# Optimization experiments

Hardware: AMD Instinct MI355X
Metric: run time of the kernel (lower is better)

## Reference

```python
import jax, jax.numpy as jnp
import numpy as np

DIM = 4096
N_HEADS = 32
HEAD_DIM = DIM // N_HEADS  # 128
B = 2
S = 2048
ADAPTER_LEN = 10
NEG_INF = -1e30


def _rope(t, cos, sin):
    # t: [B, S, H, hd]; cos/sin: [S, hd//2]
    b, s, h, d = t.shape
    tr = t.reshape(b, s, h, d // 2, 2)
    a, bb = tr[..., 0], tr[..., 1]
    c = cos[None, :, None, :]
    sn = sin[None, :, None, :]
    out = jnp.stack([a * c - bb * sn, a * sn + bb * c], axis=-1)
    return out.reshape(b, s, h, d)


def _attn(q, k, v, mask=None):
    # q: [B,H,Q,d], k/v: [B,H,K,d]
    scores = jnp.einsum('bhqd,bhkd->bhqk', q, k) / np.sqrt(HEAD_DIM).astype(q.dtype)
    if mask is not None:
        scores = scores + mask
    probs = jax.nn.softmax(scores.astype(jnp.float32), axis=-1).astype(q.dtype)
    return jnp.einsum('bhqk,bhkd->bhqd', probs, v)


def setup_inputs() -> dict:
    key = jax.random.key(0)
    ks = jax.random.split(key, 8)
    w_std = 0.02
    x = jax.random.normal(ks[0], (B, S, DIM), dtype=jnp.float32)
    wq = jax.random.normal(ks[1], (DIM, DIM), dtype=jnp.float32) * w_std
    wk = jax.random.normal(ks[2], (DIM, DIM), dtype=jnp.float32) * w_std
    wv = jax.random.normal(ks[3], (DIM, DIM), dtype=jnp.float32) * w_std
    wo = jax.random.normal(ks[4], (DIM, DIM), dtype=jnp.float32) * w_std
    gate = jax.random.normal(ks[5], (1, N_HEADS, 1, 1), dtype=jnp.float32)
    adapter = jax.random.normal(ks[6], (1, ADAPTER_LEN, DIM), dtype=jnp.float32)
    # RoPE tables (theta = 10000)
    inv_freq = 1.0 / (10000.0 ** (np.arange(0, HEAD_DIM, 2, dtype=np.float32) / HEAD_DIM))
    angles = np.outer(np.arange(S, dtype=np.float32), inv_freq)  # [S, hd//2]
    freqs_cos = jnp.asarray(np.cos(angles), dtype=jnp.float32)
    freqs_sin = jnp.asarray(np.sin(angles), dtype=jnp.float32)
    # causal additive mask [1,1,S,S]
    mask = jnp.triu(jnp.full((S, S), NEG_INF, dtype=jnp.float32), k=1)[None, None]
    return {"x": x, "wq": wq, "wk": wk, "wv": wv, "wo": wo, "gate": gate,
            "adapter": adapter, "freqs_cos": freqs_cos, "freqs_sin": freqs_sin,
            "mask": mask, "start_pos": 0}


def reference(x, wq, wk, wv, wo, gate, adapter, freqs_cos, freqs_sin, mask, start_pos):
    bsz, seqlen, _ = x.shape
    # QKV projections (torch Linear: y = x @ W.T)
    xq = jnp.einsum('bsd,ed->bse', x, wq).reshape(bsz, seqlen, N_HEADS, HEAD_DIM)
    xk = jnp.einsum('bsd,ed->bse', x, wk).reshape(bsz, seqlen, N_HEADS, HEAD_DIM)
    xv = jnp.einsum('bsd,ed->bse', x, wv).reshape(bsz, seqlen, N_HEADS, HEAD_DIM)
    xq = _rope(xq, freqs_cos, freqs_sin)
    xk = _rope(xk, freqs_cos, freqs_sin)
    # KV-cache write + read: start_pos == 0 and cache is zero-initialized, so
    # keys/values over [:start_pos+seqlen] equal the freshly written xk/xv.
    q = xq.transpose(0, 2, 1, 3)      # [B,H,S,d]
    keys = xk.transpose(0, 2, 1, 3)
    values = xv.transpose(0, 2, 1, 3)
    output = _attn(q, keys, values, mask)
    # gated adapter cross-attention
    a_k = jnp.einsum('bld,ed->ble', adapter, wk).reshape(1, ADAPTER_LEN, N_HEADS, HEAD_DIM)
    a_v = jnp.einsum('bld,ed->ble', adapter, wv).reshape(1, ADAPTER_LEN, N_HEADS, HEAD_DIM)
    a_k = jnp.broadcast_to(a_k, (bsz, ADAPTER_LEN, N_HEADS, HEAD_DIM)).transpose(0, 2, 1, 3)
    a_v = jnp.broadcast_to(a_v, (bsz, ADAPTER_LEN, N_HEADS, HEAD_DIM)).transpose(0, 2, 1, 3)
    output = output + jnp.tanh(gate) * _attn(q, a_k, a_v)
    output = output.transpose(0, 2, 1, 3).reshape(bsz, seqlen, DIM)
    return jnp.einsum('bse,de->bsd', output, wo)
```

## Files before the change

kernel.cpp:

```cpp
#include <hip/hip_runtime.h>

typedef unsigned short u16;
typedef __attribute__((ext_vector_type(8))) short short8;
typedef __attribute__((ext_vector_type(4))) float f32x4;

#define L2E   1.44269504088896340736f
#define SCALE 0.08838834764831845f
#define NEGI  -1e30f
#define WN    ((size_t)4096 * 4096)
#define TNB   ((size_t)2048 * 4096)

__device__ __forceinline__ float b2f(u16 u) {
  union { float f; unsigned int i; } v; v.i = ((unsigned int)u) << 16; return v.f;
}
__device__ __forceinline__ u16 f2b(float f) {
  union { float f; unsigned int i; } v; v.f = f;
  unsigned int r = v.i + 0x7fffu + ((v.i >> 16) & 1u);
  return (u16)(r >> 16);
}
__device__ __forceinline__ void gload16(const u16* g, u16* l) {
  __builtin_amdgcn_global_load_lds((const __attribute__((address_space(1))) void*)g,
                                   (__attribute__((address_space(3))) void*)l, 16, 0, 0);
}
__device__ __forceinline__ short8 ld8_f32_to_bf16(const float* p) {
  float4 a = *(const float4*)p;
  float4 b = *(const float4*)(p + 4);
  short8 pk;
  pk[0] = (short)f2b(a.x); pk[1] = (short)f2b(a.y);
  pk[2] = (short)f2b(a.z); pk[3] = (short)f2b(a.w);
  pk[4] = (short)f2b(b.x); pk[5] = (short)f2b(b.y);
  pk[6] = (short)f2b(b.z); pk[7] = (short)f2b(b.w);
  return pk;
}

__global__ __launch_bounds__(256) void cvt_bf16(const float* __restrict__ src,
                                                u16* __restrict__ dst)
{
  size_t e = ((size_t)blockIdx.x * 256 + threadIdx.x) * 8;
  *(short8*)(dst + e) = ld8_f32_to_bf16(src + e);
}

__global__ __launch_bounds__(256, 2) void gemm_nt(const u16* __restrict__ A,
    const u16* __restrict__ B, void* __restrict__ Cv, int mode)
{
  __shared__ __align__(16) u16 As[128 * 64];
  __shared__ __align__(16) u16 Bs[128 * 64];
  const int tid  = threadIdx.x;
  const int wave = tid >> 6, lane = tid & 63;
  const int quad = lane >> 4, l16 = lane & 15;
  const int bm = blockIdx.y * 128, bn = blockIdx.x * 128;
  const int wm = (wave >> 1) * 64, wn = (wave & 1) * 64;

  f32x4 acc[4][4];
#pragma unroll
  for (int i = 0; i < 4; i++)
#pragma unroll
    for (int j = 0; j < 4; j++) acc[i][j] = (f32x4)0.0f;

  for (int k0 = 0; k0 < 4096; k0 += 64) {
    __syncthreads();
#pragma unroll
    for (int i = 0; i < 4; i++) {
      int c = tid + i * 256;
      int row = c >> 3, cb = (c & 7) << 3;
      gload16(A + (((size_t)(bm + row)) << 12) + k0 + cb, As + c * 8);
      gload16(B + (((size_t)(bn + row)) << 12) + k0 + cb, Bs + c * 8);
    }
    __syncthreads();
#pragma unroll
    for (int ks = 0; ks < 2; ks++) {
      short8 af[4], bf[4];
#pragma unroll
      for (int t = 0; t < 4; t++) {
        af[t] = *(const short8*)(As + (wm + t * 16 + l16) * 64 + ks * 32 + quad * 8);
        bf[t] = *(const short8*)(Bs + (wn + t * 16 + l16) * 64 + ks * 32 + quad * 8);
      }
#pragma unroll
      for (int mt = 0; mt < 4; mt++)
#pragma unroll
        for (int nt = 0; nt < 4; nt++)
          acc[mt][nt] = __builtin_amdgcn_mfma_f32_16x16x32_bf16(af[mt], bf[nt], acc[mt][nt], 0, 0, 0);
    }
  }
#pragma unroll
  for (int mt = 0; mt < 4; mt++)
#pragma unroll
    for (int nt = 0; nt < 4; nt++)
#pragma unroll
      for (int r = 0; r < 4; r++) {
        int row = bm + wm + mt * 16 + quad * 4 + r;
        int col = bn + wn + nt * 16 + l16;
        float v = acc[mt][nt][r];
        if (mode == 2) {
          ((float*)Cv)[(((size_t)row) << 12) + col] = v;
        } else if (mode == 1) {
          ((u16*)Cv)[((size_t)(col >> 11)) * TNB + (((size_t)row) << 11) + (col & 2047)] = f2b(v);
        } else {
          ((u16*)Cv)[(((size_t)row) << 12) + col] = f2b(v);
        }
      }
}

__global__ __launch_bounds__(256) void rope_kernel(u16* __restrict__ Q, u16* __restrict__ K,
    const float* __restrict__ fc, const float* __restrict__ fs)
{
  int gid = blockIdx.x * 256 + threadIdx.x;
  int tsel = gid >> 21;
  int r = gid & 2097151;
  int row = r >> 9, gp = r & 511;
  int s = row & 2047;
  int e0 = gp * 8;
  int i0 = (e0 >> 1) & 63;
  u16* p = (tsel ? K : Q) + (((size_t)row) << 12) + e0;
  short8 v = *(const short8*)p;
  float4 c4 = *(const float4*)(fc + s * 64 + i0);
  float4 s4 = *(const float4*)(fs + s * 64 + i0);
  float cc[4] = {c4.x, c4.y, c4.z, c4.w};
  float ss[4] = {s4.x, s4.y, s4.z, s4.w};
  short8 w;
#pragma unroll
  for (int j = 0; j < 4; j++) {
    float a  = b2f((u16)v[2 * j]);
    float bb = b2f((u16)v[2 * j + 1]);
    w[2 * j]     = (short)f2b(a * cc[j] - bb * ss[j]);
    w[2 * j + 1] = (short)f2b(a * ss[j] + bb * cc[j]);
  }
  *(short8*)p = w;
}

__global__ __launch_bounds__(256) void adapter_kv(const float* __restrict__ adapter,
    const float* __restrict__ wk, const float* __restrict__ wv,
    u16* __restrict__ ak, u16* __restrict__ av)
{
  int gid  = blockIdx.x * 4 + (threadIdx.x >> 6);
  int lane = threadIdx.x & 63;
  int which = (gid >= 40960) ? 1 : 0;
  int rem = gid - which * 40960;
  int l = rem >> 12, col = rem & 4095;
  const float* w = which ? wv : wk;
  u16* o = which ? av : ak;
  const float* arow = adapter + l * 4096;
  const float* wrow = w + (((size_t)col) << 12);
  float sum = 0.f;
#pragma unroll
  for (int i = 0; i < 8; i++) {
    int e = i * 512 + lane * 8;
    float4 a0 = *(const float4*)(arow + e);
    float4 a1 = *(const float4*)(arow + e + 4);
    float4 w0 = *(const float4*)(wrow + e);
    float4 w1 = *(const float4*)(wrow + e + 4);
    sum += a0.x * w0.x + a0.y * w0.y + a0.z * w0.z + a0.w * w0.w
         + a1.x * w1.x + a1.y * w1.y + a1.z * w1.z + a1.w * w1.w;
  }
#pragma unroll
  for (int off = 1; off < 64; off <<= 1) sum += __shfl_xor(sum, off, 64);
  if (lane == 0) o[rem] = f2b(sum);
}

__global__ __launch_bounds__(256, 2) void flash_attn(const u16* __restrict__ Q,
    const u16* __restrict__ K, const u16* __restrict__ V, u16* __restrict__ O)
{
  Q += (size_t)blockIdx.y * TNB;
  K += (size_t)blockIdx.y * TNB;
  V += (size_t)blockIdx.y * TNB;
  O += (size_t)blockIdx.y * TNB;
  __shared__ __align__(16) u16 sm[40960];
  u16* Ps = sm + 32768;
  const int tid  = threadIdx.x;
  const int wave = tid >> 6, lane = tid & 63;
  const int quad = lane >> 4, l16 = lane & 15;
  const int qt = 15 - blockIdx.z;
  const int h  = blockIdx.x;
  const int q0 = qt * 128;
  const size_t qkBase = (size_t)h * 128;
  const size_t vBase  = ((size_t)(h * 128)) << 11;

  u16* Qs = sm + 16384;
#pragma unroll
  for (int i = 0; i < 8; i++) {
    int c = tid + i * 256;
    int row = c >> 4;
    int cb  = ((c & 15) ^ (row & 7)) << 3;
    gload16(Q + qkBase + (((size_t)(q0 + row)) << 12) + cb, Qs + c * 8);
  }
#pragma unroll
  for (int i = 0; i < 4; i++) {
    int c = tid + i * 256;
    int krow = c >> 4;
    int kcb  = ((c & 15) ^ (krow & 7)) << 3;
    gload16(K + qkBase + (((size_t)krow) << 12) + kcb, sm + c * 8);
    int vrow = c >> 3;
    int vcb  = ((c & 7) ^ (vrow & 7)) << 3;
    gload16(V + vBase + (((size_t)vrow) << 11) + vcb, sm + 8192 + c * 8);
  }
  __syncthreads();
  short8 qa[2][4];
#pragma unroll
  for (int mt = 0; mt < 2; mt++)
#pragma unroll
    for (int ks = 0; ks < 4; ks++) {
      int qr = wave * 32 + mt * 16 + l16;
      qa[mt][ks] = *(const short8*)(Qs + qr * 128 + (((ks * 4 + quad) ^ (qr & 7)) << 3));
    }
  __syncthreads();

  f32x4 acc_o[2][8];
#pragma unroll
  for (int mt = 0; mt < 2; mt++)
#pragma unroll
    for (int n = 0; n < 8; n++) acc_o[mt][n] = (f32x4)0.0f;
  float m_st[2][4], l_st[2][4];
#pragma unroll
  for (int mt = 0; mt < 2; mt++)
#pragma unroll
    for (int r = 0; r < 4; r++) { m_st[mt][r] = NEGI; l_st[mt][r] = 0.f; }

  const int qw0 = q0 + wave * 32;
  const int ntiles = 2 * (qt + 1);
  for (int t = 0; t < ntiles; t++) {
    const int kv0 = t * 64;
    u16* Kc = sm + (t & 1) * 16384;
    u16* Vc = Kc + 8192;
    if (t + 1 < ntiles) {
      const int nk = kv0 + 64;
      u16* Kn = sm + ((t + 1) & 1) * 16384;
      u16* Vn = Kn + 8192;
#pragma unroll
      for (int i = 0; i < 4; i++) {
        int c = tid + i * 256;
        int krow = c >> 4;
        int kcb  = ((c & 15) ^ (krow & 7)) << 3;
        gload16(K + qkBase + (((size_t)(nk + krow)) << 12) + kcb, Kn + c * 8);
        int vrow = c >> 3;
        int vcb  = ((c & 7) ^ (vrow & 7)) << 3;
        gload16(V + vBase + (((size_t)vrow) << 11) + nk + vcb, Vn + c * 8);
      }
    }

    if (kv0 <= qw0 + 31) {
      f32x4 sc[2][4];
#pragma unroll
      for (int mt = 0; mt < 2; mt++)
#pragma unroll
        for (int nt = 0; nt < 4; nt++) sc[mt][nt] = (f32x4)0.0f;
      __builtin_amdgcn_s_setprio(1);
#pragma unroll
      for (int ks = 0; ks < 4; ks++) {
        short8 kb[4];
#pragma unroll
        for (int nt = 0; nt < 4; nt++) {
          int kr = nt * 16 + l16;
          kb[nt] = *(const short8*)(Kc + kr * 128 + (((ks * 4 + quad) ^ (kr & 7)) << 3));
        }
#pragma unroll
        for (int mt = 0; mt < 2; mt++)
#pragma unroll
          for (int nt = 0; nt < 4; nt++)
            sc[mt][nt] = __builtin_amdgcn_mfma_f32_16x16x32_bf16(qa[mt][ks], kb[nt], sc[mt][nt], 0, 0, 0);
      }
      __builtin_amdgcn_s_setprio(0);
#pragma unroll
      for (int mt = 0; mt < 2; mt++)
#pragma unroll
        for (int nt = 0; nt < 4; nt++)
#pragma unroll
          for (int r = 0; r < 4; r++) {
            int qrow = qw0 + mt * 16 + quad * 4 + r;
            int key  = kv0 + nt * 16 + l16;
            float s = sc[mt][nt][r] * SCALE;
            sc[mt][nt][r] = (key > qrow) ? NEGI : s;
          }
      float alpha[2][4];
#pragma unroll
      for (int mt = 0; mt < 2; mt++)
#pragma unroll
        for (int r = 0; r < 4; r++) {
          float mx = fmaxf(fmaxf(sc[mt][0][r], sc[mt][1][r]), fmaxf(sc[mt][2][r], sc[mt][3][r]));
          mx = fmaxf(mx, __shfl_xor(mx, 1, 64));
          mx = fmaxf(mx, __shfl_xor(mx, 2, 64));
          mx = fmaxf(mx, __shfl_xor(mx, 4, 64));
          mx = fmaxf(mx, __shfl_xor(mx, 8, 64));
          float mnew = fmaxf(m_st[mt][r], mx);
          float al = __builtin_amdgcn_exp2f((m_st[mt][r] - mnew) * L2E);
          float rs = 0.f;
#pragma unroll
          for (int nt = 0; nt < 4; nt++) {
            float p = __builtin_amdgcn_exp2f((sc[mt][nt][r] - mnew) * L2E);
            sc[mt][nt][r] = p;
            rs += p;
          }
          rs += __shfl_xor(rs, 1, 64);
          rs += __shfl_xor(rs, 2, 64);
          rs += __shfl_xor(rs, 4, 64);
          rs += __shfl_xor(rs, 8, 64);
          l_st[mt][r] = l_st[mt][r] * al + rs;
          m_st[mt][r] = mnew;
          alpha[mt][r] = al;
        }
#pragma unroll
      for (int mt = 0; mt < 2; mt++)
#pragma unroll
        for (int n = 0; n < 8; n++)
#pragma unroll
          for (int r = 0; r < 4; r++) acc_o[mt][n][r] *= alpha[mt][r];
      u16* Pw = Ps + wave * 2048;
#pragma unroll
      for (int mt = 0; mt < 2; mt++)
#pragma unroll
        for (int nt = 0; nt < 4; nt++)
#pragma unroll
          for (int r = 0; r < 4; r++) {
            int prow = mt * 16 + quad * 4 + r;
            int pcol = nt * 16 + l16;
            Pw[prow * 64 + (((pcol >> 3) ^ (prow & 7)) << 3) + (pcol & 7)] = f2b(sc[mt][nt][r]);
          }
      __builtin_amdgcn_s_setprio(1);
#pragma unroll
      for (int ks2 = 0; ks2 < 2; ks2++) {
        short8 pa[2];
#pragma unroll
        for (int mt = 0; mt < 2; mt++) {
          int pr = mt * 16 + l16;
          pa[mt] = *(const short8*)(Pw + pr * 64 + (((ks2 * 4 + quad) ^ (pr & 7)) << 3));
        }
#pragma unroll
        for (int n = 0; n < 8; n++) {
          int vr = n * 16 + l16;
          short8 vb = *(const short8*)(Vc + vr * 64 + (((ks2 * 4 + quad) ^ (vr & 7)) << 3));
#pragma unroll
          for (int mt = 0; mt < 2; mt++)
            acc_o[mt][n] = __builtin_amdgcn_mfma_f32_16x16x32_bf16(pa[mt], vb, acc_o[mt][n], 0, 0, 0);
        }
      }
      __builtin_amdgcn_s_setprio(0);
    }
    __syncthreads();
  }
#pragma unroll
  for (int mt = 0; mt < 2; mt++)
#pragma unroll
    for (int r = 0; r < 4; r++) {
      float inv = 1.0f / l_st[mt][r];
      int qrow = qw0 + mt * 16 + quad * 4 + r;
#pragma unroll
      for (int n = 0; n < 8; n++) {
        int d = n * 16 + l16;
        O[qkBase + (((size_t)qrow) << 12) + d] = f2b(acc_o[mt][n][r] * inv);
      }
    }
}

__global__ __launch_bounds__(256) void adapter_attn(const u16* __restrict__ Q,
    const u16* __restrict__ ak, const u16* __restrict__ av,
    const float* __restrict__ gate, u16* __restrict__ AO)
{
  int gid  = blockIdx.x * 4 + (threadIdx.x >> 6);
  int lane = threadIdx.x & 63;
  int row = gid >> 5, h = gid & 31;
  float g = tanhf(gate[h]);
  const u16* qp = Q + (((size_t)row) << 12) + h * 128 + lane * 2;
  float qa = b2f(qp[0]), qb = b2f(qp[1]);
  float p[10];
#pragma unroll
  for (int l = 0; l < 10; l++) {
    const u16* kp = ak + l * 4096 + h * 128 + lane * 2;
    p[l] = qa * b2f(kp[0]) + qb * b2f(kp[1]);
  }
#pragma unroll
  for (int l = 0; l < 10; l++)
#pragma unroll
    for (int off = 1; off < 64; off <<= 1) p[l] += __shfl_xor(p[l], off, 64);
  float m = NEGI;
#pragma unroll
  for (int l = 0; l < 10; l++) { p[l] *= SCALE; m = fmaxf(m, p[l]); }
  float sum = 0.f;
#pragma unroll
  for (int l = 0; l < 10; l++) { p[l] = __builtin_amdgcn_exp2f((p[l] - m) * L2E); sum += p[l]; }
  float gi = g / sum;
  float a0 = 0.f, a1 = 0.f;
#pragma unroll
  for (int l = 0; l < 10; l++) {
    const u16* vp = av + l * 4096 + h * 128 + lane * 2;
    a0 += p[l] * b2f(vp[0]);
    a1 += p[l] * b2f(vp[1]);
  }
  u16* op = AO + (((size_t)row) << 12) + h * 128 + lane * 2;
  op[0] = f2b(b2f(op[0]) + gi * a0);
  op[1] = f2b(b2f(op[1]) + gi * a1);
}

extern "C" void kernel_launch(void* const* d_in, const int* in_sizes, int n_in,
                              void* d_out, int out_size, void* d_ws, size_t ws_size,
                              hipStream_t stream) {
  (void)in_sizes; (void)n_in; (void)out_size; (void)ws_size;
  const float* x       = (const float*)d_in[0];
  const float* wq      = (const float*)d_in[1];
  const float* wk      = (const float*)d_in[2];
  const float* wv      = (const float*)d_in[3];
  const float* wo      = (const float*)d_in[4];
  const float* gate    = (const float*)d_in[5];
  const float* adapter = (const float*)d_in[6];
  const float* fc      = (const float*)d_in[7];
  const float* fs      = (const float*)d_in[8];
  float* out = (float*)d_out;

  u16* wb  = (u16*)d_ws;
  u16* xb  = wb + WN;
  u16* Qf  = xb + WN;
  u16* Kf  = Qf + WN;
  u16* Vtf = Kf + WN;
  u16* AOf = xb;
  u16* ak  = Vtf + WN;
  u16* av  = ak + 40960;

  adapter_kv<<<20480, 256, 0, stream>>>(adapter, wk, wv, ak, av);
  cvt_bf16<<<8192, 256, 0, stream>>>(x, xb);

  cvt_bf16<<<8192, 256, 0, stream>>>(wq, wb);
  gemm_nt<<<dim3(32, 32), 256, 0, stream>>>(xb, wb, Qf, 0);
  cvt_bf16<<<8192, 256, 0, stream>>>(wk, wb);
  gemm_nt<<<dim3(32, 32), 256, 0, stream>>>(xb, wb, Kf, 0);
  cvt_bf16<<<8192, 256, 0, stream>>>(wv, wb);
  gemm_nt<<<dim3(32, 32), 256, 0, stream>>>(wb, xb, Vtf, 1);

  rope_kernel<<<16384, 256, 0, stream>>>(Qf, Kf, fc, fs);
  flash_attn<<<dim3(32, 2, 16), 256, 0, stream>>>(Qf, Kf, Vtf, AOf);
  adapter_attn<<<32768, 256, 0, stream>>>(Qf, ak, av, gate, AOf);

  cvt_bf16<<<8192, 256, 0, stream>>>(wo, wb);
  gemm_nt<<<dim3(32, 32), 256, 0, stream>>>(AOf, wb, out, 2);
}
```

Measured before the change: 1.488 ms.

## Double-buffer GEMM LDS tiles and XOR-swizzle to avoid bank conflicts

The bf16 NT GEMM now uses two LDS buffers per operand, issuing global-to-LDS loads for the next K tile while MFMAs run on the current one. A single barrier per iteration replaces the two. The LDS column chunks are also XOR-swizzled by row so the 16-byte fragment reads spread across banks. LDS use doubles to 64KB per block, which may limit the intended two blocks per CU. Correctness depends on the vmcnt wait placed before the barrier covering the async loads.

```diff
diff --git a/kernel.cpp b/kernel.cpp
--- a/kernel.cpp
+++ b/kernel.cpp
@@ -43,8 +43,8 @@
 __global__ __launch_bounds__(256, 2) void gemm_nt(const u16* __restrict__ A,
     const u16* __restrict__ B, void* __restrict__ Cv, int mode)
 {
-  __shared__ __align__(16) u16 As[128 * 64];
-  __shared__ __align__(16) u16 Bs[128 * 64];
+  __shared__ __align__(16) u16 As[2][128 * 64];
+  __shared__ __align__(16) u16 Bs[2][128 * 64];
   const int tid  = threadIdx.x;
   const int wave = tid >> 6, lane = tid & 63;
   const int quad = lane >> 4, l16 = lane & 15;
@@ -57,23 +57,38 @@
 #pragma unroll
     for (int j = 0; j < 4; j++) acc[i][j] = (f32x4)0.0f;
 
-  for (int k0 = 0; k0 < 4096; k0 += 64) {
-    __syncthreads();
-#pragma unroll
-    for (int i = 0; i < 4; i++) {
-      int c = tid + i * 256;
-      int row = c >> 3, cb = (c & 7) << 3;
-      gload16(A + (((size_t)(bm + row)) << 12) + k0 + cb, As + c * 8);
-      gload16(B + (((size_t)(bn + row)) << 12) + k0 + cb, Bs + c * 8);
-    }
-    __syncthreads();
+#pragma unroll
+  for (int i = 0; i < 4; i++) {
+    int c = tid + i * 256;
+    int row = c >> 3;
+    int cb  = ((c & 7) ^ (row & 7)) << 3;
+    gload16(A + (((size_t)(bm + row)) << 12) + cb, As[0] + c * 8);
+    gload16(B + (((size_t)(bn + row)) << 12) + cb, Bs[0] + c * 8);
+  }
+  __syncthreads();
+
+  for (int t = 0; t < 64; t++) {
+    const int bi = t & 1;
+    if (t < 63) {
+      const int k0 = (t + 1) * 64;
+#pragma unroll
+      for (int i = 0; i < 4; i++) {
+        int c = tid + i * 256;
+        int row = c >> 3;
+        int cb  = ((c & 7) ^ (row & 7)) << 3;
+        gload16(A + (((size_t)(bm + row)) << 12) + k0 + cb, As[bi ^ 1] + c * 8);
+        gload16(B + (((size_t)(bn + row)) << 12) + k0 + cb, Bs[bi ^ 1] + c * 8);
+      }
+    }
 #pragma unroll
     for (int ks = 0; ks < 2; ks++) {
       short8 af[4], bf[4];
 #pragma unroll
-      for (int t = 0; t < 4; t++) {
-        af[t] = *(const short8*)(As + (wm + t * 16 + l16) * 64 + ks * 32 + quad * 8);
-        bf[t] = *(const short8*)(Bs + (wn + t * 16 + l16) * 64 + ks * 32 + quad * 8);
+      for (int tt = 0; tt < 4; tt++) {
+        int ar = wm + tt * 16 + l16;
+        int br = wn + tt * 16 + l16;
+        af[tt] = *(const short8*)(As[bi] + ar * 64 + (((ks * 4 + quad) ^ (ar & 7)) << 3));
+        bf[tt] = *(const short8*)(Bs[bi] + br * 64 + (((ks * 4 + quad) ^ (br & 7)) << 3));
       }
 #pragma unroll
       for (int mt = 0; mt < 4; mt++)
@@ -81,6 +96,7 @@
         for (int nt = 0; nt < 4; nt++)
           acc[mt][nt] = __builtin_amdgcn_mfma_f32_16x16x32_bf16(af[mt], bf[nt], acc[mt][nt], 0, 0, 0);
     }
+    __syncthreads();
   }
 #pragma unroll
   for (int mt = 0; mt < 4; mt++)
```

Result: no change. 1.486 ms (-0.1%).
